# Kernel optimization log

Hardware: AMD Instinct MI355X
Metric: run time of the kernel (lower is better)

The kernel has to match this reference:

```python
import jax, jax.numpy as jnp
import numpy as np

# bi-degrees (0,0),(1,0),(0,1),(1,1) -> d = (2a+1)*(2b+1)
DEG_DIMS = [1, 3, 3, 9]
P, C = 8192, 256


def setup_inputs() -> dict:
    key = jax.random.key(0)
    kx, k0, k1, k2 = jax.random.split(key, 4)
    scale = 1.0 / np.sqrt(C).astype(np.float32)
    x = jax.random.normal(kx, (P, C, sum(DEG_DIMS)), dtype=jnp.float32)
    # torch.randn(mo, mi) / sqrt(mi); W10 is shared by degrees (1,0) and (0,1)
    W00 = jax.random.normal(k0, (C, C), dtype=jnp.float32) * scale
    W10 = jax.random.normal(k1, (C, C), dtype=jnp.float32) * scale
    W11 = jax.random.normal(k2, (C, C), dtype=jnp.float32) * scale
    return {"x": x, "W00": W00, "W10": W10, "W11": W11}


def reference(x, W00, W10, W11):
    # Weight for each degree segment; (0,1) reuses W10 (parameter tying in GLinear)
    Ws = [W00, W10, W10, W11]
    offsets = np.concatenate([[0], np.cumsum(DEG_DIMS)])
    outs = []
    for W, a, b in zip(Ws, offsets[:-1], offsets[1:]):
        v = x[:, :, a:b]                      # (p, c_in, d_k)
        outs.append(jnp.einsum('oi,pid->pod', W, v))
    out = jnp.concatenate(outs, axis=-1)      # (p, c_out, sum_d)
    # use_skip with matching shared channel -> residual add of input
    return out + x
```

## Files before the change

kernel.cpp:

```cpp
#include <hip/hip_runtime.h>
#include <hip/hip_bf16.h>


#define C_DIM   256
#define D_DIM   16
#define P_TILE  16
#define KC      64
#define LDS_ROW 72

typedef __attribute__((ext_vector_type(8))) short  short8v;
typedef __attribute__((ext_vector_type(4))) float  float4v;
typedef __attribute__((ext_vector_type(4))) unsigned int uint4v;

__device__ __forceinline__ unsigned int pack_bf16x2_rne(float lo, float hi) {
    unsigned int ul = __builtin_bit_cast(unsigned int, lo);
    unsigned int uh = __builtin_bit_cast(unsigned int, hi);
    ul = (ul + 0x7fffu + ((ul >> 16) & 1u)) >> 16;
    uh = (uh + 0x7fffu + ((uh >> 16) & 1u));
    return (ul & 0xffffu) | (uh & 0xffff0000u);
}

__device__ __forceinline__ unsigned int pack_bf16x2_tr(float lo, float hi) {
    return __builtin_amdgcn_perm(__builtin_bit_cast(unsigned int, hi),
                                 __builtin_bit_cast(unsigned int, lo),
                                 0x07060302u);
}

__device__ __forceinline__ short8v load_w_frag(const float* __restrict__ W, int row, int col) {
    const float* p = W + (size_t)row * C_DIM + col;
    float4v a = *(const float4v*)p;
    float4v b = *(const float4v*)(p + 4);
    uint4v u;
    u.x = pack_bf16x2_tr(a.x, a.y);
    u.y = pack_bf16x2_tr(a.z, a.w);
    u.z = pack_bf16x2_tr(b.x, b.y);
    u.w = pack_bf16x2_tr(b.z, b.w);
    return __builtin_bit_cast(short8v, u);
}

__global__ __launch_bounds__(512, 1) void glinear_kernel(
    const float* __restrict__ x, const float* __restrict__ W00,
    const float* __restrict__ W10, const float* __restrict__ W11,
    float* __restrict__ out)
{
    __shared__ __align__(16) unsigned short ls[P_TILE * D_DIM * LDS_ROW];

    const int t    = threadIdx.x;
    const int lane = t & 63;
    const int w    = t >> 6;
    const int lm   = lane & 15;
    const int quad = lane >> 4;

    const int pbase = blockIdx.x * P_TILE;

    float4v acc[2][16];
    const float4v fzero = {0.f, 0.f, 0.f, 0.f};
    #pragma unroll
    for (int a = 0; a < 2; ++a)
        #pragma unroll
        for (int b = 0; b < 16; ++b) acc[a][b] = fzero;

    const int d4    = t & 3;
    const int ip    = (t >> 2) & 31;
    const int pq    = t >> 7;
    const int i_loc = ip * 2;

    const int orow0 = w * 32 + lm;
    const int orow1 = w * 32 + 16 + lm;

    for (int ic = 0; ic < 4; ++ic) {
        const int ibase = ic * KC;

        #pragma unroll
        for (int it = 0; it < 4; ++it) {
            const int p = pq + it * 4;
            const float* src = x + ((size_t)(pbase + p) * C_DIM + (ibase + i_loc)) * D_DIM + d4 * 4;
            float4v a = *(const float4v*)src;
            float4v b = *(const float4v*)(src + D_DIM);
            const int g = (i_loc >> 3) ^ (p & 7);
            const int e = i_loc & 7;
            const int base = (p * D_DIM + d4 * 4) * LDS_ROW + g * 8 + e;
            #pragma unroll
            for (int dj = 0; dj < 4; ++dj) {
                *(unsigned int*)(&ls[base + dj * LDS_ROW]) = pack_bf16x2_rne(a[dj], b[dj]);
            }
        }
        __syncthreads();

        #pragma unroll
        for (int ks = 0; ks < 2; ++ks) {
            const int col = ibase + ks * 32 + quad * 8;
            const int gq  = ((ks * 4 + quad) ^ (lm & 7));
            const unsigned short* brow = &ls[lm * D_DIM * LDS_ROW + gq * 8];

            short8v f00_0 = load_w_frag(W00, orow0, col);
            short8v f00_1 = load_w_frag(W00, orow1, col);
            short8v f10_0 = load_w_frag(W10, orow0, col);
            short8v f10_1 = load_w_frag(W10, orow1, col);
            short8v f11_0 = load_w_frag(W11, orow0, col);
            short8v f11_1 = load_w_frag(W11, orow1, col);

            #pragma unroll
            for (int dd = 0; dd < 16; ++dd) {
                short8v xf = *(const short8v*)(brow + dd * LDS_ROW);
                short8v w0 = (dd == 0) ? f00_0 : (dd <= 6) ? f10_0 : f11_0;
                short8v w1 = (dd == 0) ? f00_1 : (dd <= 6) ? f10_1 : f11_1;
                acc[0][dd] = __builtin_amdgcn_mfma_f32_16x16x32_bf16(xf, w0, acc[0][dd], 0, 0, 0);
                acc[1][dd] = __builtin_amdgcn_mfma_f32_16x16x32_bf16(xf, w1, acc[1][dd], 0, 0, 0);
            }
        }
        __syncthreads();
    }

    #pragma unroll
    for (int ot = 0; ot < 2; ++ot) {
        const int o = w * 32 + ot * 16 + lm;
        #pragma unroll
        for (int r = 0; r < 4; ++r) {
            const int p = pbase + quad * 4 + r;
            const size_t off = (size_t)p * (C_DIM * D_DIM) + (size_t)o * D_DIM;
            #pragma unroll
            for (int g = 0; g < 4; ++g) {
                float4v v;
                v.x = acc[ot][g * 4 + 0][r];
                v.y = acc[ot][g * 4 + 1][r];
                v.z = acc[ot][g * 4 + 2][r];
                v.w = acc[ot][g * 4 + 3][r];
                float4v xr = *(const float4v*)(x + off + g * 4);
                *(float4v*)(out + off + g * 4) = v + xr;
            }
        }
    }
}

extern "C" void kernel_launch(void* const* d_in, const int* in_sizes, int n_in,
                              void* d_out, int out_size, void* d_ws, size_t ws_size,
                              hipStream_t stream) {
    const float* x   = (const float*)d_in[0];
    const float* W00 = (const float*)d_in[1];
    const float* W10 = (const float*)d_in[2];
    const float* W11 = (const float*)d_in[3];
    float* out = (float*)d_out;

    dim3 grid(512);
    dim3 block(512);
    hipLaunchKernelGGL(glinear_kernel, grid, block, 0, stream, x, W00, W10, W11, out);
}
```

Measured before the change: 314.5 us.

## Prefetch next x chunk into LDS via global_load_lds with double-buffered bf16 tiles

```diff
diff --git a/kernel.cpp b/kernel.cpp
--- a/kernel.cpp
+++ b/kernel.cpp
@@ -38,12 +38,20 @@
     return __builtin_bit_cast(short8v, u);
 }
 
-__global__ __launch_bounds__(512, 1) void glinear_kernel(
+__device__ __forceinline__ void glds16(const float* g, float* l) {
+    __builtin_amdgcn_global_load_lds(
+        (const __attribute__((address_space(1))) void*)g,
+        (__attribute__((address_space(3))) void*)l,
+        16, 0, 0);
+}
+
+__global__ __launch_bounds__(512, 2) void glinear_kernel(
     const float* __restrict__ x, const float* __restrict__ W00,
     const float* __restrict__ W10, const float* __restrict__ W11,
     float* __restrict__ out)
 {
-    __shared__ __align__(16) unsigned short ls[P_TILE * D_DIM * LDS_ROW];
+    __shared__ __align__(16) float f32s[64 * 256];
+    __shared__ __align__(16) unsigned short ls[2][P_TILE * D_DIM * LDS_ROW];
 
     const int t    = threadIdx.x;
     const int lane = t & 63;
@@ -68,30 +76,47 @@
     const int orow0 = w * 32 + lm;
     const int orow1 = w * 32 + 16 + lm;
 
+    auto stage_chunk = [&](int ic) {
+        #pragma unroll
+        for (int it = 0; it < 4; ++it) {
+            const float* src = x + ((size_t)(pbase + pq + it * 4) * C_DIM
+                                    + (ic * KC + i_loc)) * D_DIM + d4 * 4;
+            glds16(src,         &f32s[((it * 2 + 0) * 8 + w) << 8]);
+            glds16(src + D_DIM, &f32s[((it * 2 + 1) * 8 + w) << 8]);
+        }
+    };
+
+    stage_chunk(0);
+
     for (int ic = 0; ic < 4; ++ic) {
         const int ibase = ic * KC;
+        const int ib    = ic & 1;
+
+        asm volatile("s_waitcnt vmcnt(0)" ::: "memory");
 
         #pragma unroll
         for (int it = 0; it < 4; ++it) {
             const int p = pq + it * 4;
-            const float* src = x + ((size_t)(pbase + p) * C_DIM + (ibase + i_loc)) * D_DIM + d4 * 4;
-            float4v a = *(const float4v*)src;
-            float4v b = *(const float4v*)(src + D_DIM);
+            float4v a = *(const float4v*)&f32s[((((it * 2 + 0) * 8 + w) << 8)) + lane * 4];
+            float4v b = *(const float4v*)&f32s[((((it * 2 + 1) * 8 + w) << 8)) + lane * 4];
             const int g = (i_loc >> 3) ^ (p & 7);
             const int e = i_loc & 7;
             const int base = (p * D_DIM + d4 * 4) * LDS_ROW + g * 8 + e;
             #pragma unroll
             for (int dj = 0; dj < 4; ++dj) {
-                *(unsigned int*)(&ls[base + dj * LDS_ROW]) = pack_bf16x2_rne(a[dj], b[dj]);
+                *(unsigned int*)(&ls[ib][base + dj * LDS_ROW]) = pack_bf16x2_rne(a[dj], b[dj]);
             }
         }
         __syncthreads();
+
+        if (ic < 3) stage_chunk(ic + 1);
+        asm volatile("" ::: "memory");
 
         #pragma unroll
         for (int ks = 0; ks < 2; ++ks) {
             const int col = ibase + ks * 32 + quad * 8;
             const int gq  = ((ks * 4 + quad) ^ (lm & 7));
-            const unsigned short* brow = &ls[lm * D_DIM * LDS_ROW + gq * 8];
+            const unsigned short* brow = &ls[ib][lm * D_DIM * LDS_ROW + gq * 8];
 
             short8v f00_0 = load_w_frag(W00, orow0, col);
             short8v f00_1 = load_w_frag(W00, orow1, col);
@@ -109,7 +134,6 @@
                 acc[1][dd] = __builtin_amdgcn_mfma_f32_16x16x32_bf16(xf, w1, acc[1][dd], 0, 0, 0);
             }
         }
-        __syncthreads();
     }
 
     #pragma unroll
@@ -127,7 +151,7 @@
                 v.z = acc[ot][g * 4 + 2][r];
                 v.w = acc[ot][g * 4 + 3][r];
                 float4v xr = *(const float4v*)(x + off + g * 4);
-                *(float4v*)(out + off + g * 4) = v + xr;
+                __builtin_nontemporal_store(v + xr, (float4v*)(out + off + g * 4));
             }
         }
     }
```

New measurement: 447.7 us. 1.42x slower.
